# Kernel tuning notes

Hardware: AMD Instinct MI355X
Metric: run time of the kernel (lower is better)

## Reference

```python
import jax, jax.numpy as jnp
import numpy as np

N_NODES = 55
N_FEAT = 48
BATCH = 16384


def _norm_adj():
    # tridiagonal adjacency with self-loops, row-normalized by degree
    i = jnp.arange(N_NODES)
    A = (jnp.abs(i[:, None] - i[None, :]) <= 1).astype(jnp.float32)  # [55,55]
    return A / A.sum(axis=1, keepdims=True)  # D^{-1} A


def setup_inputs() -> dict:
    key = jax.random.key(0)
    k1, k2, k3 = jax.random.split(key, 3)
    x = jax.random.normal(k1, (BATCH, N_NODES, N_FEAT), dtype=jnp.float32)
    W = jax.random.normal(k2, (N_FEAT, N_FEAT), dtype=jnp.float32) * (1.0 / np.sqrt(N_FEAT))
    b = jax.random.normal(k3, (N_FEAT,), dtype=jnp.float32) * 0.01
    return {"x": x, "W": W, "b": b}


def reference(x, W, b):
    DA = _norm_adj()                                  # [55,55]
    AX = jnp.einsum('ij,bjf->bif', DA, x)             # banded neighbor avg
    # nn.Linear: y = AX @ W^T + b, then ReLU
    return jax.nn.relu(jnp.einsum('bif,of->bio', AX, W) + b)
```

## Files before the change

### kernel.cpp

```cpp
#include <hip/hip_runtime.h>


#define NODES 55
#define F 48
#define BT 4
#define ROWS 224
#define ST 56

typedef __attribute__((ext_vector_type(8))) short short8_t;
typedef __attribute__((ext_vector_type(4))) float floatx4;

__device__ __forceinline__ unsigned short f2bf(float f) {
    union { float f; unsigned int u; } v; v.f = f;
    unsigned int u = v.u;
    u += 0x7FFFu + ((u >> 16) & 1u);
    return (unsigned short)(u >> 16);
}

__global__ __launch_bounds__(256, 4)
void gconv_kernel(const float* __restrict__ x, const float* __restrict__ W,
                  const float* __restrict__ bias, float* __restrict__ out) {
    __shared__ unsigned short s_ax[ROWS * ST];
    __shared__ unsigned short s_w[F * ST];

    const int tid = threadIdx.x;
    const int b0 = blockIdx.x * BT;

    if (tid >= 240) {
        int i = tid - 240;
        for (int t = i; t < 48; t += 16) {
            int row = 220 + (t / 12), c = t - (t / 12) * 12;
            *(uint2*)&s_ax[row * ST + c * 4] = make_uint2(0u, 0u);
        }
    }

    for (int i = tid; i < F * F; i += 256) {
        int o = i / 48, f = i - o * 48;
        s_w[o * ST + f] = f2bf(W[i]);
    }

    if (tid < 240) {
        const int s   = tid / 48;
        const int rem = tid - s * 48;
        const int b_l = rem / 12;
        const int fq  = rem - b_l * 12;
        const float4* xg = reinterpret_cast<const float4*>(x);
        const int base = (b0 + b_l) * (NODES * 12) + fq;
        const int n0 = s * 11;

        float4 v[13];
#pragma unroll
        for (int t = 0; t < 13; ++t) {
            int n = n0 - 1 + t;
            int nc = n < 0 ? 0 : (n > 54 ? 54 : n);
            float4 tmp = xg[base + nc * 12];
            bool ok = (n >= 0) & (n <= 54);
            v[t].x = ok ? tmp.x : 0.f;
            v[t].y = ok ? tmp.y : 0.f;
            v[t].z = ok ? tmp.z : 0.f;
            v[t].w = ok ? tmp.w : 0.f;
        }

#pragma unroll
        for (int t = 0; t < 11; ++t) {
            int n = n0 + t;
            float w = (n == 0 || n == 54) ? 0.5f : (1.0f / 3.0f);
            float sx = (v[t].x + v[t + 1].x + v[t + 2].x) * w;
            float sy = (v[t].y + v[t + 1].y + v[t + 2].y) * w;
            float sz = (v[t].z + v[t + 1].z + v[t + 2].z) * w;
            float sw = (v[t].w + v[t + 1].w + v[t + 2].w) * w;
            unsigned int lo = (unsigned int)f2bf(sx) | ((unsigned int)f2bf(sy) << 16);
            unsigned int hi = (unsigned int)f2bf(sz) | ((unsigned int)f2bf(sw) << 16);
            *(uint2*)&s_ax[(n * BT + b_l) * ST + fq * 4] = make_uint2(lo, hi);
        }
    }
    __syncthreads();

    const int lane = tid & 63;
    const int wave = tid >> 6;
    const int col  = lane & 15;
    const int quad = lane >> 4;

    const short8_t zero8 = {0, 0, 0, 0, 0, 0, 0, 0};

    short8_t wf[3][2];
#pragma unroll
    for (int nt = 0; nt < 3; ++nt) {
        wf[nt][0] = *(const short8_t*)&s_w[(nt * 16 + col) * ST + quad * 8];
        short8_t t1 = *(const short8_t*)&s_w[(nt * 16 + col) * ST + 32 + (quad & 1) * 8];
        wf[nt][1] = (quad < 2) ? t1 : zero8;
    }

    floatx4 bv[3];
#pragma unroll
    for (int mt = 0; mt < 3; ++mt)
        bv[mt] = *(const floatx4*)&bias[mt * 16 + quad * 4];

    for (int m = wave; m < 14; m += 4) {
        const int nb = m * 16 + col;
        short8_t a0 = *(const short8_t*)&s_ax[nb * ST + quad * 8];
        short8_t t1 = *(const short8_t*)&s_ax[nb * ST + 32 + (quad & 1) * 8];
        short8_t a1 = (quad < 2) ? t1 : zero8;

        floatx4 acc0 = {0.f, 0.f, 0.f, 0.f};
        floatx4 acc1 = {0.f, 0.f, 0.f, 0.f};
        floatx4 acc2 = {0.f, 0.f, 0.f, 0.f};
        acc0 = __builtin_amdgcn_mfma_f32_16x16x32_bf16(wf[0][0], a0, acc0, 0, 0, 0);
        acc1 = __builtin_amdgcn_mfma_f32_16x16x32_bf16(wf[1][0], a0, acc1, 0, 0, 0);
        acc2 = __builtin_amdgcn_mfma_f32_16x16x32_bf16(wf[2][0], a0, acc2, 0, 0, 0);
        acc0 = __builtin_amdgcn_mfma_f32_16x16x32_bf16(wf[0][1], a1, acc0, 0, 0, 0);
        acc1 = __builtin_amdgcn_mfma_f32_16x16x32_bf16(wf[1][1], a1, acc1, 0, 0, 0);
        acc2 = __builtin_amdgcn_mfma_f32_16x16x32_bf16(wf[2][1], a1, acc2, 0, 0, 0);

        const int node = nb >> 2;
        const int b_l  = nb & 3;
        if (node < NODES) {
            float* op = out + ((b0 + b_l) * NODES + node) * F + quad * 4;
            floatx4 v0 = acc0 + bv[0];
            floatx4 v1 = acc1 + bv[1];
            floatx4 v2 = acc2 + bv[2];
#pragma unroll
            for (int j = 0; j < 4; ++j) {
                v0[j] = v0[j] > 0.f ? v0[j] : 0.f;
                v1[j] = v1[j] > 0.f ? v1[j] : 0.f;
                v2[j] = v2[j] > 0.f ? v2[j] : 0.f;
            }
            *(floatx4*)(op)      = v0;
            *(floatx4*)(op + 16) = v1;
            *(floatx4*)(op + 32) = v2;
        }
    }
}

extern "C" void kernel_launch(void* const* d_in, const int* in_sizes, int n_in,
                              void* d_out, int out_size, void* d_ws, size_t ws_size,
                              hipStream_t stream) {
    const float* x    = (const float*)d_in[0];
    const float* W    = (const float*)d_in[1];
    const float* bias = (const float*)d_in[2];
    float* out = (float*)d_out;
    const int BATCH = 16384;
    dim3 grid(BATCH / BT);
    dim3 block(256);
    gconv_kernel<<<grid, block, 0, stream>>>(x, W, bias, out);
}
```

Before: 297.9 us.

## Drop LDS staging; compute neighbor average directly from global loads into MFMA fragments

Removes shared-memory staging of the aggregated features and weights along with the block barrier. Each lane now loads its three neighbor rows of x straight from global memory, averages and packs them to bf16 in registers, and feeds the MFMA. Weight fragments are likewise loaded and converted per lane from global memory. In exchange, x is read three times per row (relying on caches), the fixed four-iteration loop adds padded idle work, and occupancy hints drop from 4 to 3 blocks.

```diff
diff --git a/kernel.cpp b/kernel.cpp
--- a/kernel.cpp
+++ b/kernel.cpp
@@ -4,8 +4,6 @@
 #define NODES 55
 #define F 48
 #define BT 4
-#define ROWS 224
-#define ST 56
 
 typedef __attribute__((ext_vector_type(8))) short short8_t;
 typedef __attribute__((ext_vector_type(4))) float floatx4;
@@ -17,90 +15,85 @@
     return (unsigned short)(u >> 16);
 }
 
-__global__ __launch_bounds__(256, 4)
+__device__ __forceinline__ short8_t pack8(floatx4 lo, floatx4 hi) {
+    short8_t r;
+    r[0] = (short)f2bf(lo[0]); r[1] = (short)f2bf(lo[1]);
+    r[2] = (short)f2bf(lo[2]); r[3] = (short)f2bf(lo[3]);
+    r[4] = (short)f2bf(hi[0]); r[5] = (short)f2bf(hi[1]);
+    r[6] = (short)f2bf(hi[2]); r[7] = (short)f2bf(hi[3]);
+    return r;
+}
+
+__global__ __launch_bounds__(256, 3)
 void gconv_kernel(const float* __restrict__ x, const float* __restrict__ W,
                   const float* __restrict__ bias, float* __restrict__ out) {
-    __shared__ unsigned short s_ax[ROWS * ST];
-    __shared__ unsigned short s_w[F * ST];
-
-    const int tid = threadIdx.x;
-    const int b0 = blockIdx.x * BT;
-
-    if (tid >= 240) {
-        int i = tid - 240;
-        for (int t = i; t < 48; t += 16) {
-            int row = 220 + (t / 12), c = t - (t / 12) * 12;
-            *(uint2*)&s_ax[row * ST + c * 4] = make_uint2(0u, 0u);
-        }
-    }
-
-    for (int i = tid; i < F * F; i += 256) {
-        int o = i / 48, f = i - o * 48;
-        s_w[o * ST + f] = f2bf(W[i]);
-    }
-
-    if (tid < 240) {
-        const int s   = tid / 48;
-        const int rem = tid - s * 48;
-        const int b_l = rem / 12;
-        const int fq  = rem - b_l * 12;
-        const float4* xg = reinterpret_cast<const float4*>(x);
-        const int base = (b0 + b_l) * (NODES * 12) + fq;
-        const int n0 = s * 11;
-
-        float4 v[13];
-#pragma unroll
-        for (int t = 0; t < 13; ++t) {
-            int n = n0 - 1 + t;
-            int nc = n < 0 ? 0 : (n > 54 ? 54 : n);
-            float4 tmp = xg[base + nc * 12];
-            bool ok = (n >= 0) & (n <= 54);
-            v[t].x = ok ? tmp.x : 0.f;
-            v[t].y = ok ? tmp.y : 0.f;
-            v[t].z = ok ? tmp.z : 0.f;
-            v[t].w = ok ? tmp.w : 0.f;
-        }
-
-#pragma unroll
-        for (int t = 0; t < 11; ++t) {
-            int n = n0 + t;
-            float w = (n == 0 || n == 54) ? 0.5f : (1.0f / 3.0f);
-            float sx = (v[t].x + v[t + 1].x + v[t + 2].x) * w;
-            float sy = (v[t].y + v[t + 1].y + v[t + 2].y) * w;
-            float sz = (v[t].z + v[t + 1].z + v[t + 2].z) * w;
-            float sw = (v[t].w + v[t + 1].w + v[t + 2].w) * w;
-            unsigned int lo = (unsigned int)f2bf(sx) | ((unsigned int)f2bf(sy) << 16);
-            unsigned int hi = (unsigned int)f2bf(sz) | ((unsigned int)f2bf(sw) << 16);
-            *(uint2*)&s_ax[(n * BT + b_l) * ST + fq * 4] = make_uint2(lo, hi);
-        }
-    }
-    __syncthreads();
-
+    const int tid  = threadIdx.x;
     const int lane = tid & 63;
     const int wave = tid >> 6;
     const int col  = lane & 15;
     const int quad = lane >> 4;
+    const int b0   = blockIdx.x * BT;
 
+    const int ko1 = 32 + (quad & 1) * 8;
     const short8_t zero8 = {0, 0, 0, 0, 0, 0, 0, 0};
 
     short8_t wf[3][2];
 #pragma unroll
     for (int nt = 0; nt < 3; ++nt) {
-        wf[nt][0] = *(const short8_t*)&s_w[(nt * 16 + col) * ST + quad * 8];
-        short8_t t1 = *(const short8_t*)&s_w[(nt * 16 + col) * ST + 32 + (quad & 1) * 8];
-        wf[nt][1] = (quad < 2) ? t1 : zero8;
+        const float* wr = W + (nt * 16 + col) * F;
+        floatx4 w0 = *(const floatx4*)(wr + quad * 8);
+        floatx4 w1 = *(const floatx4*)(wr + quad * 8 + 4);
+        floatx4 w2 = *(const floatx4*)(wr + ko1);
+        floatx4 w3 = *(const floatx4*)(wr + ko1 + 4);
+        wf[nt][0] = pack8(w0, w1);
+        short8_t t = pack8(w2, w3);
+        wf[nt][1] = (quad < 2) ? t : zero8;
     }
 
     floatx4 bv[3];
 #pragma unroll
-    for (int mt = 0; mt < 3; ++mt)
-        bv[mt] = *(const floatx4*)&bias[mt * 16 + quad * 4];
+    for (int nt = 0; nt < 3; ++nt)
+        bv[nt] = *(const floatx4*)&bias[nt * 16 + quad * 4];
 
-    for (int m = wave; m < 14; m += 4) {
-        const int nb = m * 16 + col;
-        short8_t a0 = *(const short8_t*)&s_ax[nb * ST + quad * 8];
-        short8_t t1 = *(const short8_t*)&s_ax[nb * ST + 32 + (quad & 1) * 8];
-        short8_t a1 = (quad < 2) ? t1 : zero8;
+#pragma unroll 2
+    for (int it = 0; it < 4; ++it) {
+        const int m    = wave + it * 4;
+        const int nb   = m * 16 + col;
+        const int node = nb >> 2;
+        const int b_l  = nb & 3;
+
+        int nm = node - 1; nm = nm < 0 ? 0 : (nm > 54 ? 54 : nm);
+        int nc = node;     nc = nc > 54 ? 54 : nc;
+        int np = node + 1; np = np > 54 ? 54 : np;
+
+        const float ONE3 = 0.33333333333333333f;
+        const float wl = (node == 0) ? 0.0f : ((node >= 54) ? 0.5f : ONE3);
+        const float wm = (node == 0 || node >= 54) ? 0.5f : ONE3;
+        const float wr_ = (node == 0) ? 0.5f : ((node >= 54) ? 0.0f : ONE3);
+
+        const float* r0 = x + ((b0 + b_l) * NODES + nm) * F;
+        const float* r1 = x + ((b0 + b_l) * NODES + nc) * F;
+        const float* r2 = x + ((b0 + b_l) * NODES + np) * F;
+
+        floatx4 X00 = *(const floatx4*)(r0 + quad * 8);
+        floatx4 X01 = *(const floatx4*)(r0 + quad * 8 + 4);
+        floatx4 X02 = *(const floatx4*)(r0 + ko1);
+        floatx4 X03 = *(const floatx4*)(r0 + ko1 + 4);
+        floatx4 X10 = *(const floatx4*)(r1 + quad * 8);
+        floatx4 X11 = *(const floatx4*)(r1 + quad * 8 + 4);
+        floatx4 X12 = *(const floatx4*)(r1 + ko1);
+        floatx4 X13 = *(const floatx4*)(r1 + ko1 + 4);
+        floatx4 X20 = *(const floatx4*)(r2 + quad * 8);
+        floatx4 X21 = *(const floatx4*)(r2 + quad * 8 + 4);
+        floatx4 X22 = *(const floatx4*)(r2 + ko1);
+        floatx4 X23 = *(const floatx4*)(r2 + ko1 + 4);
+
+        floatx4 A0a = wl * X00 + wm * X10 + wr_ * X20;
+        floatx4 A0b = wl * X01 + wm * X11 + wr_ * X21;
+        floatx4 A1a = wl * X02 + wm * X12 + wr_ * X22;
+        floatx4 A1b = wl * X03 + wm * X13 + wr_ * X23;
+        short8_t a0 = pack8(A0a, A0b);
+        short8_t a1 = pack8(A1a, A1b);
 
         floatx4 acc0 = {0.f, 0.f, 0.f, 0.f};
         floatx4 acc1 = {0.f, 0.f, 0.f, 0.f};
@@ -112,8 +105,6 @@
         acc1 = __builtin_amdgcn_mfma_f32_16x16x32_bf16(wf[1][1], a1, acc1, 0, 0, 0);
         acc2 = __builtin_amdgcn_mfma_f32_16x16x32_bf16(wf[2][1], a1, acc2, 0, 0, 0);
 
-        const int node = nb >> 2;
-        const int b_l  = nb & 3;
         if (node < NODES) {
             float* op = out + ((b0 + b_l) * NODES + node) * F + quad * 4;
             floatx4 v0 = acc0 + bv[0];
```

Result: slower. 359.6 us (+20.7%).

## Make blocks persistent over several tiles with double-buffered LDS prefetch

Applied to the files above, without the earlier changes.

Each block now handles eight batch tiles instead of one, with a grid of 512 blocks. The global loads for the next tile are issued before computing the current tile, and the smoothed data is written into a second LDS buffer. The W conversion and setup are amortized across tiles, and load latency should overlap with the MFMA compute and stores. In exchange, occupancy drops (launch bounds 4 to 2, doubled LDS), only 512 blocks exist, and the prefetch registers v[13] stay live across compute.

```diff
diff --git a/kernel.cpp b/kernel.cpp
--- a/kernel.cpp
+++ b/kernel.cpp
@@ -6,6 +6,8 @@
 #define BT 4
 #define ROWS 224
 #define ST 56
+#define TPB 8
+#define NBLOCKS 512
 
 typedef __attribute__((ext_vector_type(8))) short short8_t;
 typedef __attribute__((ext_vector_type(4))) float floatx4;
@@ -17,20 +19,19 @@
     return (unsigned short)(u >> 16);
 }
 
-__global__ __launch_bounds__(256, 4)
+__global__ __launch_bounds__(256, 2)
 void gconv_kernel(const float* __restrict__ x, const float* __restrict__ W,
                   const float* __restrict__ bias, float* __restrict__ out) {
-    __shared__ unsigned short s_ax[ROWS * ST];
+    __shared__ unsigned short s_ax[2][ROWS * ST];
     __shared__ unsigned short s_w[F * ST];
 
     const int tid = threadIdx.x;
-    const int b0 = blockIdx.x * BT;
 
-    if (tid >= 240) {
-        int i = tid - 240;
-        for (int t = i; t < 48; t += 16) {
-            int row = 220 + (t / 12), c = t - (t / 12) * 12;
-            *(uint2*)&s_ax[row * ST + c * 4] = make_uint2(0u, 0u);
+    if (tid >= 224) {
+        for (int t = tid - 224; t < 96; t += 32) {
+            int bu = t / 48, r = t - bu * 48;
+            int row = 220 + r / 12, c = r - (r / 12) * 12;
+            *(uint2*)&s_ax[bu][row * ST + c * 4] = make_uint2(0u, 0u);
         }
     }
 
@@ -39,48 +40,56 @@
         s_w[o * ST + f] = f2bf(W[i]);
     }
 
-    if (tid < 240) {
-        const int s   = tid / 48;
-        const int rem = tid - s * 48;
-        const int b_l = rem / 12;
-        const int fq  = rem - b_l * 12;
-        const float4* xg = reinterpret_cast<const float4*>(x);
-        const int base = (b0 + b_l) * (NODES * 12) + fq;
-        const int n0 = s * 11;
+    const bool is_stager = tid < 240;
+    const int s   = tid / 48;
+    const int rem = tid - s * 48;
+    const int sb  = rem / 12;
+    const int fq  = rem - sb * 12;
+    const int n0  = s * 11;
+    const float4* xg = reinterpret_cast<const float4*>(x);
 
-        float4 v[13];
+    float4 v[13];
+
+    const int tile0 = blockIdx.x * TPB;
+
+    auto stage_load = [&](int tile) {
+        if (!is_stager) return;
+        const int base = (tile * BT + sb) * (NODES * 12) + fq;
 #pragma unroll
         for (int t = 0; t < 13; ++t) {
             int n = n0 - 1 + t;
             int nc = n < 0 ? 0 : (n > 54 ? 54 : n);
-            float4 tmp = xg[base + nc * 12];
-            bool ok = (n >= 0) & (n <= 54);
-            v[t].x = ok ? tmp.x : 0.f;
-            v[t].y = ok ? tmp.y : 0.f;
-            v[t].z = ok ? tmp.z : 0.f;
-            v[t].w = ok ? tmp.w : 0.f;
+            v[t] = xg[base + nc * 12];
         }
+    };
 
+    auto smooth_write = [&](int bu) {
+        if (!is_stager) return;
+        const float ONE3 = 0.33333333333333333f;
 #pragma unroll
         for (int t = 0; t < 11; ++t) {
             int n = n0 + t;
-            float w = (n == 0 || n == 54) ? 0.5f : (1.0f / 3.0f);
-            float sx = (v[t].x + v[t + 1].x + v[t + 2].x) * w;
-            float sy = (v[t].y + v[t + 1].y + v[t + 2].y) * w;
-            float sz = (v[t].z + v[t + 1].z + v[t + 2].z) * w;
-            float sw = (v[t].w + v[t + 1].w + v[t + 2].w) * w;
+            float wl = (n == 0) ? 0.0f : ((n == 54) ? 0.5f : ONE3);
+            float wm = (n == 0 || n == 54) ? 0.5f : ONE3;
+            float wr = (n == 54) ? 0.0f : ((n == 0) ? 0.5f : ONE3);
+            float sx = v[t].x * wl + v[t + 1].x * wm + v[t + 2].x * wr;
+            float sy = v[t].y * wl + v[t + 1].y * wm + v[t + 2].y * wr;
+            float sz = v[t].z * wl + v[t + 1].z * wm + v[t + 2].z * wr;
+            float sw = v[t].w * wl + v[t + 1].w * wm + v[t + 2].w * wr;
             unsigned int lo = (unsigned int)f2bf(sx) | ((unsigned int)f2bf(sy) << 16);
             unsigned int hi = (unsigned int)f2bf(sz) | ((unsigned int)f2bf(sw) << 16);
-            *(uint2*)&s_ax[(n * BT + b_l) * ST + fq * 4] = make_uint2(lo, hi);
+            *(uint2*)&s_ax[bu][(n * BT + sb) * ST + fq * 4] = make_uint2(lo, hi);
         }
-    }
+    };
+
+    stage_load(tile0);
+    smooth_write(0);
     __syncthreads();
 
     const int lane = tid & 63;
     const int wave = tid >> 6;
     const int col  = lane & 15;
     const int quad = lane >> 4;
-
     const short8_t zero8 = {0, 0, 0, 0, 0, 0, 0, 0};
 
     short8_t wf[3][2];
@@ -90,44 +99,55 @@
         short8_t t1 = *(const short8_t*)&s_w[(nt * 16 + col) * ST + 32 + (quad & 1) * 8];
         wf[nt][1] = (quad < 2) ? t1 : zero8;
     }
-
     floatx4 bv[3];
 #pragma unroll
     for (int mt = 0; mt < 3; ++mt)
         bv[mt] = *(const floatx4*)&bias[mt * 16 + quad * 4];
 
-    for (int m = wave; m < 14; m += 4) {
-        const int nb = m * 16 + col;
-        short8_t a0 = *(const short8_t*)&s_ax[nb * ST + quad * 8];
-        short8_t t1 = *(const short8_t*)&s_ax[nb * ST + 32 + (quad & 1) * 8];
-        short8_t a1 = (quad < 2) ? t1 : zero8;
+    auto compute = [&](int bu, int tile) {
+        const int b0 = tile * BT;
+        for (int m = wave; m < 14; m += 4) {
+            const int nb = m * 16 + col;
+            short8_t a0 = *(const short8_t*)&s_ax[bu][nb * ST + quad * 8];
+            short8_t t1 = *(const short8_t*)&s_ax[bu][nb * ST + 32 + (quad & 1) * 8];
+            short8_t a1 = (quad < 2) ? t1 : zero8;
 
-        floatx4 acc0 = {0.f, 0.f, 0.f, 0.f};
-        floatx4 acc1 = {0.f, 0.f, 0.f, 0.f};
-        floatx4 acc2 = {0.f, 0.f, 0.f, 0.f};
-        acc0 = __builtin_amdgcn_mfma_f32_16x16x32_bf16(wf[0][0], a0, acc0, 0, 0, 0);
-        acc1 = __builtin_amdgcn_mfma_f32_16x16x32_bf16(wf[1][0], a0, acc1, 0, 0, 0);
-        acc2 = __builtin_amdgcn_mfma_f32_16x16x32_bf16(wf[2][0], a0, acc2, 0, 0, 0);
-        acc0 = __builtin_amdgcn_mfma_f32_16x16x32_bf16(wf[0][1], a1, acc0, 0, 0, 0);
-        acc1 = __builtin_amdgcn_mfma_f32_16x16x32_bf16(wf[1][1], a1, acc1, 0, 0, 0);
-        acc2 = __builtin_amdgcn_mfma_f32_16x16x32_bf16(wf[2][1], a1, acc2, 0, 0, 0);
+            floatx4 acc0 = {0.f, 0.f, 0.f, 0.f};
+            floatx4 acc1 = {0.f, 0.f, 0.f, 0.f};
+            floatx4 acc2 = {0.f, 0.f, 0.f, 0.f};
+            acc0 = __builtin_amdgcn_mfma_f32_16x16x32_bf16(wf[0][0], a0, acc0, 0, 0, 0);
+            acc1 = __builtin_amdgcn_mfma_f32_16x16x32_bf16(wf[1][0], a0, acc1, 0, 0, 0);
+            acc2 = __builtin_amdgcn_mfma_f32_16x16x32_bf16(wf[2][0], a0, acc2, 0, 0, 0);
+            acc0 = __builtin_amdgcn_mfma_f32_16x16x32_bf16(wf[0][1], a1, acc0, 0, 0, 0);
+            acc1 = __builtin_amdgcn_mfma_f32_16x16x32_bf16(wf[1][1], a1, acc1, 0, 0, 0);
+            acc2 = __builtin_amdgcn_mfma_f32_16x16x32_bf16(wf[2][1], a1, acc2, 0, 0, 0);
 
-        const int node = nb >> 2;
-        const int b_l  = nb & 3;
-        if (node < NODES) {
-            float* op = out + ((b0 + b_l) * NODES + node) * F + quad * 4;
-            floatx4 v0 = acc0 + bv[0];
-            floatx4 v1 = acc1 + bv[1];
-            floatx4 v2 = acc2 + bv[2];
+            const int node = nb >> 2;
+            const int b_l  = nb & 3;
+            if (node < NODES) {
+                float* op = out + ((b0 + b_l) * NODES + node) * F + quad * 4;
+                floatx4 v0 = acc0 + bv[0];
+                floatx4 v1 = acc1 + bv[1];
+                floatx4 v2 = acc2 + bv[2];
 #pragma unroll
-            for (int j = 0; j < 4; ++j) {
-                v0[j] = v0[j] > 0.f ? v0[j] : 0.f;
-                v1[j] = v1[j] > 0.f ? v1[j] : 0.f;
-                v2[j] = v2[j] > 0.f ? v2[j] : 0.f;
+                for (int j = 0; j < 4; ++j) {
+                    v0[j] = v0[j] > 0.f ? v0[j] : 0.f;
+                    v1[j] = v1[j] > 0.f ? v1[j] : 0.f;
+                    v2[j] = v2[j] > 0.f ? v2[j] : 0.f;
+                }
+                *(floatx4*)(op)      = v0;
+                *(floatx4*)(op + 16) = v1;
+                *(floatx4*)(op + 32) = v2;
             }
-            *(floatx4*)(op)      = v0;
-            *(floatx4*)(op + 16) = v1;
-            *(floatx4*)(op + 32) = v2;
+        }
+    };
+
+    for (int t = 0; t < TPB; ++t) {
+        if (t + 1 < TPB) stage_load(tile0 + t + 1);
+        compute(t & 1, tile0 + t);
+        if (t + 1 < TPB) {
+            smooth_write((t + 1) & 1);
+            __syncthreads();
         }
     }
 }
@@ -139,8 +159,7 @@
     const float* W    = (const float*)d_in[1];
     const float* bias = (const float*)d_in[2];
     float* out = (float*)d_out;
-    const int BATCH = 16384;
-    dim3 grid(BATCH / BT);
+    dim3 grid(NBLOCKS);
     dim3 block(256);
     gconv_kernel<<<grid, block, 0, stream>>>(x, W, bias, out);
 }
```

After: 320.0 us. 1.07x slower.

## Give each wave its own batch items and prefetch the next while computing

Applied to the files above, without the earlier changes.

Restructures the kernel so each wave owns a private LDS tile and handles 4 batch items in sequence. The next item's x rows are loaded into registers while MFMA and stores run on the current one, and all __syncthreads are removed. W is converted straight from global memory into register fragments, dropping the shared W staging. The grid shrinks to 1024 blocks, which gives fewer, longer-lived blocks and raises register pressure from the 13-entry prefetch buffer held across compute; this may reduce occupancy. The wave-private LDS tile is written and read without any explicit wave-level barrier.

```diff
diff --git a/kernel.cpp b/kernel.cpp
--- a/kernel.cpp
+++ b/kernel.cpp
@@ -3,9 +3,9 @@
 
 #define NODES 55
 #define F 48
-#define BT 4
-#define ROWS 224
 #define ST 56
+#define BPW 4
+#define NBLK 1024
 
 typedef __attribute__((ext_vector_type(8))) short short8_t;
 typedef __attribute__((ext_vector_type(4))) float floatx4;
@@ -17,41 +17,65 @@
     return (unsigned short)(u >> 16);
 }
 
+__device__ __forceinline__ short8_t pack8(floatx4 lo, floatx4 hi) {
+    short8_t r;
+    r[0] = (short)f2bf(lo[0]); r[1] = (short)f2bf(lo[1]);
+    r[2] = (short)f2bf(lo[2]); r[3] = (short)f2bf(lo[3]);
+    r[4] = (short)f2bf(hi[0]); r[5] = (short)f2bf(hi[1]);
+    r[6] = (short)f2bf(hi[2]); r[7] = (short)f2bf(hi[3]);
+    return r;
+}
+
 __global__ __launch_bounds__(256, 4)
 void gconv_kernel(const float* __restrict__ x, const float* __restrict__ W,
                   const float* __restrict__ bias, float* __restrict__ out) {
-    __shared__ unsigned short s_ax[ROWS * ST];
-    __shared__ unsigned short s_w[F * ST];
+    __shared__ __align__(16) unsigned short s_ax[4][56 * ST];
 
-    const int tid = threadIdx.x;
-    const int b0 = blockIdx.x * BT;
+    const int tid  = threadIdx.x;
+    const int lane = tid & 63;
+    const int wave = tid >> 6;
+    unsigned short* sl = &s_ax[wave][0];
 
-    if (tid >= 240) {
-        int i = tid - 240;
-        for (int t = i; t < 48; t += 16) {
-            int row = 220 + (t / 12), c = t - (t / 12) * 12;
-            *(uint2*)&s_ax[row * ST + c * 4] = make_uint2(0u, 0u);
-        }
+    if (lane < 14) *(uint2*)&sl[55 * ST + lane * 4] = make_uint2(0u, 0u);
+
+    const int col  = lane & 15;
+    const int quad = lane >> 4;
+    const int ko1  = 32 + (quad & 1) * 8;
+    const short8_t zero8 = {0, 0, 0, 0, 0, 0, 0, 0};
+
+    short8_t wf[3][2];
+#pragma unroll
+    for (int nt = 0; nt < 3; ++nt) {
+        const float* wr = W + (nt * 16 + col) * F;
+        floatx4 w0 = *(const floatx4*)(wr + quad * 8);
+        floatx4 w1 = *(const floatx4*)(wr + quad * 8 + 4);
+        floatx4 w2 = *(const floatx4*)(wr + ko1);
+        floatx4 w3 = *(const floatx4*)(wr + ko1 + 4);
+        wf[nt][0] = pack8(w0, w1);
+        short8_t t = pack8(w2, w3);
+        wf[nt][1] = (quad < 2) ? t : zero8;
     }
+    floatx4 bv[3];
+#pragma unroll
+    for (int nt = 0; nt < 3; ++nt)
+        bv[nt] = *(const floatx4*)&bias[nt * 16 + quad * 4];
 
-    for (int i = tid; i < F * F; i += 256) {
-        int o = i / 48, f = i - o * 48;
-        s_w[o * ST + f] = f2bf(W[i]);
-    }
+    const bool stager = lane < 60;
+    const int s  = lane / 12;
+    const int fq = lane - s * 12;
+    const int n0 = s * 11;
+    const float4* xg = reinterpret_cast<const float4*>(x);
 
-    if (tid < 240) {
-        const int s   = tid / 48;
-        const int rem = tid - s * 48;
-        const int b_l = rem / 12;
-        const int fq  = rem - b_l * 12;
-        const float4* xg = reinterpret_cast<const float4*>(x);
-        const int base = (b0 + b_l) * (NODES * 12) + fq;
-        const int n0 = s * 11;
+    float4 v[13];
 
-        float4 v[13];
+    const int bbase = (blockIdx.x * 4 + wave) * BPW;
+
+    auto load_b = [&](int b) {
+        if (!stager) return;
+        const int base = b * 660 + fq;
 #pragma unroll
         for (int t = 0; t < 13; ++t) {
-            int n = n0 - 1 + t;
+            int n  = n0 - 1 + t;
             int nc = n < 0 ? 0 : (n > 54 ? 54 : n);
             float4 tmp = xg[base + nc * 12];
             bool ok = (n >= 0) & (n <= 54);
@@ -60,75 +84,69 @@
             v[t].z = ok ? tmp.z : 0.f;
             v[t].w = ok ? tmp.w : 0.f;
         }
+    };
 
+    auto smooth_b = [&]() {
+        if (!stager) return;
+        const float ONE3 = 0.33333333333333333f;
 #pragma unroll
         for (int t = 0; t < 11; ++t) {
             int n = n0 + t;
-            float w = (n == 0 || n == 54) ? 0.5f : (1.0f / 3.0f);
+            float w = (n == 0 || n == 54) ? 0.5f : ONE3;
             float sx = (v[t].x + v[t + 1].x + v[t + 2].x) * w;
             float sy = (v[t].y + v[t + 1].y + v[t + 2].y) * w;
             float sz = (v[t].z + v[t + 1].z + v[t + 2].z) * w;
             float sw = (v[t].w + v[t + 1].w + v[t + 2].w) * w;
             unsigned int lo = (unsigned int)f2bf(sx) | ((unsigned int)f2bf(sy) << 16);
             unsigned int hi = (unsigned int)f2bf(sz) | ((unsigned int)f2bf(sw) << 16);
-            *(uint2*)&s_ax[(n * BT + b_l) * ST + fq * 4] = make_uint2(lo, hi);
+            *(uint2*)&sl[n * ST + fq * 4] = make_uint2(lo, hi);
         }
-    }
-    __syncthreads();
+    };
 
-    const int lane = tid & 63;
-    const int wave = tid >> 6;
-    const int col  = lane & 15;
-    const int quad = lane >> 4;
+    auto compute_b = [&](int b) {
+#pragma unroll
+        for (int m = 0; m < 4; ++m) {
+            const int nb = m * 16 + col;
+            const int nr = nb < 55 ? nb : 55;
+            short8_t a0 = *(const short8_t*)&sl[nr * ST + quad * 8];
+            short8_t t1 = *(const short8_t*)&sl[nr * ST + ko1];
+            short8_t a1 = (quad < 2) ? t1 : zero8;
 
-    const short8_t zero8 = {0, 0, 0, 0, 0, 0, 0, 0};
+            floatx4 acc0 = {0.f, 0.f, 0.f, 0.f};
+            floatx4 acc1 = {0.f, 0.f, 0.f, 0.f};
+            floatx4 acc2 = {0.f, 0.f, 0.f, 0.f};
+            acc0 = __builtin_amdgcn_mfma_f32_16x16x32_bf16(wf[0][0], a0, acc0, 0, 0, 0);
+            acc1 = __builtin_amdgcn_mfma_f32_16x16x32_bf16(wf[1][0], a0, acc1, 0, 0, 0);
+            acc2 = __builtin_amdgcn_mfma_f32_16x16x32_bf16(wf[2][0], a0, acc2, 0, 0, 0);
+            acc0 = __builtin_amdgcn_mfma_f32_16x16x32_bf16(wf[0][1], a1, acc0, 0, 0, 0);
+            acc1 = __builtin_amdgcn_mfma_f32_16x16x32_bf16(wf[1][1], a1, acc1, 0, 0, 0);
+            acc2 = __builtin_amdgcn_mfma_f32_16x16x32_bf16(wf[2][1], a1, acc2, 0, 0, 0);
 
-    short8_t wf[3][2];
+            if (nb < NODES) {
+                float* op = out + (b * NODES + nb) * F + quad * 4;
+                floatx4 v0 = acc0 + bv[0];
+                floatx4 v1 = acc1 + bv[1];
+                floatx4 v2 = acc2 + bv[2];
 #pragma unroll
-    for (int nt = 0; nt < 3; ++nt) {
-        wf[nt][0] = *(const short8_t*)&s_w[(nt * 16 + col) * ST + quad * 8];
-        short8_t t1 = *(const short8_t*)&s_w[(nt * 16 + col) * ST + 32 + (quad & 1) * 8];
-        wf[nt][1] = (quad < 2) ? t1 : zero8;
-    }
+                for (int j = 0; j < 4; ++j) {
+                    v0[j] = v0[j] > 0.f ? v0[j] : 0.f;
+                    v1[j] = v1[j] > 0.f ? v1[j] : 0.f;
+                    v2[j] = v2[j] > 0.f ? v2[j] : 0.f;
+                }
+                *(floatx4*)(op)      = v0;
+                *(floatx4*)(op + 16) = v1;
+                *(floatx4*)(op + 32) = v2;
+            }
+        }
+    };
 
-    floatx4 bv[3];
+    load_b(bbase);
+    smooth_b();
 #pragma unroll
-    for (int mt = 0; mt < 3; ++mt)
-        bv[mt] = *(const floatx4*)&bias[mt * 16 + quad * 4];
-
-    for (int m = wave; m < 14; m += 4) {
-        const int nb = m * 16 + col;
-        short8_t a0 = *(const short8_t*)&s_ax[nb * ST + quad * 8];
-        short8_t t1 = *(const short8_t*)&s_ax[nb * ST + 32 + (quad & 1) * 8];
-        short8_t a1 = (quad < 2) ? t1 : zero8;
-
-        floatx4 acc0 = {0.f, 0.f, 0.f, 0.f};
-        floatx4 acc1 = {0.f, 0.f, 0.f, 0.f};
-        floatx4 acc2 = {0.f, 0.f, 0.f, 0.f};
-        acc0 = __builtin_amdgcn_mfma_f32_16x16x32_bf16(wf[0][0], a0, acc0, 0, 0, 0);
-        acc1 = __builtin_amdgcn_mfma_f32_16x16x32_bf16(wf[1][0], a0, acc1, 0, 0, 0);
-        acc2 = __builtin_amdgcn_mfma_f32_16x16x32_bf16(wf[2][0], a0, acc2, 0, 0, 0);
-        acc0 = __builtin_amdgcn_mfma_f32_16x16x32_bf16(wf[0][1], a1, acc0, 0, 0, 0);
-        acc1 = __builtin_amdgcn_mfma_f32_16x16x32_bf16(wf[1][1], a1, acc1, 0, 0, 0);
-        acc2 = __builtin_amdgcn_mfma_f32_16x16x32_bf16(wf[2][1], a1, acc2, 0, 0, 0);
-
-        const int node = nb >> 2;
-        const int b_l  = nb & 3;
-        if (node < NODES) {
-            float* op = out + ((b0 + b_l) * NODES + node) * F + quad * 4;
-            floatx4 v0 = acc0 + bv[0];
-            floatx4 v1 = acc1 + bv[1];
-            floatx4 v2 = acc2 + bv[2];
-#pragma unroll
-            for (int j = 0; j < 4; ++j) {
-                v0[j] = v0[j] > 0.f ? v0[j] : 0.f;
-                v1[j] = v1[j] > 0.f ? v1[j] : 0.f;
-                v2[j] = v2[j] > 0.f ? v2[j] : 0.f;
-            }
-            *(floatx4*)(op)      = v0;
-            *(floatx4*)(op + 16) = v1;
-            *(floatx4*)(op + 32) = v2;
-        }
+    for (int j = 0; j < BPW; ++j) {
+        if (j + 1 < BPW) load_b(bbase + j + 1);
+        compute_b(bbase + j);
+        if (j + 1 < BPW) smooth_b();
     }
 }
 
@@ -139,8 +157,7 @@
     const float* W    = (const float*)d_in[1];
     const float* bias = (const float*)d_in[2];
     float* out = (float*)d_out;
-    const int BATCH = 16384;
-    dim3 grid(BATCH / BT);
+    dim3 grid(NBLK);
     dim3 block(256);
     gconv_kernel<<<grid, block, 0, stream>>>(x, W, bias, out);
 }
```

New measurement: 441.0 us. 48.0% more time.
